# Performance work log

Hardware: AMD Instinct MI355X
Metric: run time of the kernel (lower is better)

The kernel has to match this reference:

```python
import jax, jax.numpy as jnp
import numpy as np

LAMBDA_WEIGHT = 1.0


def _soft_argmax(logits):
    # differentiable_argmax: sum_c softmax(logits)[c] * c along class dim
    nc = logits.shape[1]
    probs = jax.nn.softmax(logits, axis=1)
    idx = jnp.arange(nc, dtype=logits.dtype)[None, :, None, None]
    return jnp.sum(probs * idx, axis=1)  # [B, H, W]


def _pair_loss(mask, d):
    # mask: [L] bool over row-major flattened HxW; d: [L] float (col - row).
    # torch.where returns row-major order, coord[:,1]-coord[:,0] == d at masked
    # pixels; second diff is |d_i - d_prev| over consecutive masked pixels.
    L = mask.shape[0]
    pos = jnp.where(mask, jnp.arange(L), -1)
    last = jax.lax.cummax(pos, axis=0)                 # last masked index <= i
    prev = jnp.concatenate([jnp.full((1,), -1), last[:-1]])  # strictly before i
    valid = mask & (prev >= 0)
    dprev = d[jnp.clip(prev, 0, L - 1)]
    s = jnp.sum(jnp.where(valid, jnp.abs(d - dprev), 0.0))
    npairs = jnp.sum(valid)
    npts = jnp.sum(mask)
    mean = s / jnp.maximum(npairs, 1).astype(d.dtype)
    # N==0 contributes 0 (the `continue`); N==1 gives an empty-mean (NaN) in
    # torch -- guarded to 0 here (such degenerate classes are skipped).
    return jnp.where(npts >= 2, mean / (npts + 1).astype(d.dtype), 0.0)


def reference(logits, labels):
    bs, nc, h, w = logits.shape
    seg = jnp.floor(jax.lax.stop_gradient(_soft_argmax(logits))).astype(jnp.int32)
    seg = seg.reshape(bs, h * w)                       # [B, L] row-major
    # d[i] = col - row for flattened index i
    i = jnp.arange(h * w)
    d = ((i % w) - (i // w)).astype(jnp.float32)       # [L]
    classes = jnp.arange(1, nc, dtype=jnp.int32)       # skip background c=0
    masks = seg[:, None, :] == classes[None, :, None]  # [B, nc-1, L]
    per = jax.vmap(jax.vmap(_pair_loss, in_axes=(0, None)), in_axes=(0, None))(masks, d)
    return jnp.sum(per) * LAMBDA_WEIGHT


def setup_inputs() -> dict:
    key = jax.random.key(0)
    k1, k2 = jax.random.split(key)
    logits = jax.random.normal(k1, (16, 7, 368, 640), dtype=jnp.float32)
    labels = jax.random.randint(k2, (16, 368, 640), 0, 7, dtype=jnp.int64)
    return {"logits": logits, "labels": labels}
```

## Files before the change

kernel.cpp:

```cpp
#include <hip/hip_runtime.h>
#include <cstdint>
#include <cstddef>

#define BB 16
#define CC 7
#define HH 368
#define WW 640
#define LL (HH * WW)
#define NCLS 6
#define NCOMBO (BB * NCLS)
#define PXB 1024
#define BPB (LL / PXB)
#define NBLK (BB * BPB)

struct St { int S, cnt, first, last; };

__device__ inline St comb(const St& a, const St& b) {
    if (a.cnt == 0) return b;
    if (b.cnt == 0) return a;
    St r;
    r.S     = a.S + b.S + abs(b.first - a.last);
    r.cnt   = a.cnt + b.cnt;
    r.first = a.first;
    r.last  = b.last;
    return r;
}

__global__ __launch_bounds__(256) void fused_kernel(const float* __restrict__ logits,
                                                    int4* __restrict__ blkStates) {
    int blk = blockIdx.x;
    int b  = blk / BPB;
    int bb = blk - b * BPB;
    int t  = threadIdx.x;
    int i  = bb * PXB + t * 4;
    const float* base = logits + (size_t)b * CC * LL + i;

    float x[CC][4];
#pragma unroll
    for (int c = 0; c < CC; ++c) {
        float4 v = *reinterpret_cast<const float4*>(base + (size_t)c * LL);
        x[c][0] = v.x; x[c][1] = v.y; x[c][2] = v.z; x[c][3] = v.w;
    }

    int row = i / WW;
    int col = i - row * WW;
    int d0  = col - row;

    St st[NCLS];
#pragma unroll
    for (int c = 0; c < NCLS; ++c) { st[c].S = 0; st[c].cnt = 0; st[c].first = 0; st[c].last = 0; }

#pragma unroll
    for (int k = 0; k < 4; ++k) {
        float m = x[0][k];
#pragma unroll
        for (int c = 1; c < CC; ++c) m = fmaxf(m, x[c][k]);
        float s = 0.0f, w = 0.0f;
#pragma unroll
        for (int c = 0; c < CC; ++c) {
            float e = __expf(x[c][k] - m);
            s += e;
            w += e * (float)c;
        }
        int sv = (int)floorf(__fdividef(w, s));
        int d  = d0 + k;
#pragma unroll
        for (int c = 0; c < NCLS; ++c) {
            if (sv == c + 1) {
                if (st[c].cnt == 0) st[c].first = d;
                else                st[c].S += abs(d - st[c].last);
                st[c].last = d;
                st[c].cnt++;
            }
        }
    }

    __shared__ int4 red[NCLS][256];
#pragma unroll
    for (int c = 0; c < NCLS; ++c)
        red[c][t] = make_int4(st[c].S, st[c].cnt, st[c].first, st[c].last);
    __syncthreads();

    for (int step = 1; step < 256; step <<= 1) {
        if ((t & (2 * step - 1)) == 0) {
#pragma unroll
            for (int c = 0; c < NCLS; ++c) {
                int4 A = red[c][t], B = red[c][t + step];
                St a{A.x, A.y, A.z, A.w}, bs{B.x, B.y, B.z, B.w};
                St r = comb(a, bs);
                red[c][t] = make_int4(r.S, r.cnt, r.first, r.last);
            }
        }
        __syncthreads();
    }

    if (t < NCLS) blkStates[(size_t)blk * NCLS + t] = red[t][0];
}

__global__ __launch_bounds__(256) void combine_kernel(const int4* __restrict__ blkStates,
                                                      float* __restrict__ out) {
    int combo = blockIdx.x;
    int b = combo / NCLS;
    int c = combo - b * NCLS;
    int t = threadIdx.x;

    St st{0, 0, 0, 0};
    if (t < BPB) {
        int4 v = blkStates[(size_t)(b * BPB + t) * NCLS + c];
        st = St{v.x, v.y, v.z, v.w};
    }

    __shared__ int4 red[256];
    red[t] = make_int4(st.S, st.cnt, st.first, st.last);
    __syncthreads();

    for (int step = 1; step < 256; step <<= 1) {
        if ((t & (2 * step - 1)) == 0) {
            int4 A = red[t], B = red[t + step];
            St a{A.x, A.y, A.z, A.w}, bs{B.x, B.y, B.z, B.w};
            St r = comb(a, bs);
            red[t] = make_int4(r.S, r.cnt, r.first, r.last);
        }
        __syncthreads();
    }

    if (t == 0) {
        int n = red[0].y;
        if (n >= 2) {
            double res = ((double)red[0].x / (double)(n - 1)) / (double)(n + 1);
            atomicAdd(out, (float)res);
        }
    }
}

extern "C" void kernel_launch(void* const* d_in, const int* in_sizes, int n_in,
                              void* d_out, int out_size, void* d_ws, size_t ws_size,
                              hipStream_t stream) {
    const float* logits = (const float*)d_in[0];
    float* out = (float*)d_out;

    int4* blkStates = (int4*)d_ws;

    hipMemsetAsync(out, 0, sizeof(float) * out_size, stream);
    fused_kernel<<<NBLK, 256, 0, stream>>>(logits, blkStates);
    combine_kernel<<<NCOMBO, 256, 0, stream>>>(blkStates, out);
}
```

Baseline: 171.5 us.

## Replace shared-memory tree reductions with wavefront shuffle reductions and 16 px/thread

Each thread now processes 16 pixels with 64-thread blocks (one wavefront), and the per-class segment states are reduced with __shfl_down instead of a shared-memory tree with repeated __syncthreads. The block-state layout becomes class-major, and combine_kernel also uses shuffle reduction plus a small cross-wave step. This removes the LDS traffic and barrier overhead that dominated a memory-light kernel. The trade-off is strided per-thread loads, which may reduce coalescing.

Measured after the change: 201.5 us. +17.5%, slower.

```diff
diff --git a/kernel.cpp b/kernel.cpp
--- a/kernel.cpp
+++ b/kernel.cpp
@@ -9,38 +9,41 @@
 #define LL (HH * WW)
 #define NCLS 6
 #define NCOMBO (BB * NCLS)
-#define PXB 1024
+#define PXT 16
+#define TPB 64
+#define PXB (PXT * TPB)
 #define BPB (LL / PXB)
 #define NBLK (BB * BPB)
 
 struct St { int S, cnt, first, last; };
 
 __device__ inline St comb(const St& a, const St& b) {
-    if (a.cnt == 0) return b;
-    if (b.cnt == 0) return a;
     St r;
-    r.S     = a.S + b.S + abs(b.first - a.last);
+    int both = (a.cnt > 0) & (b.cnt > 0);
+    r.S     = a.S + b.S + (both ? abs(b.first - a.last) : 0);
     r.cnt   = a.cnt + b.cnt;
-    r.first = a.first;
-    r.last  = b.last;
+    r.first = (a.cnt > 0) ? a.first : b.first;
+    r.last  = (b.cnt > 0) ? b.last : a.last;
     return r;
 }
 
-__global__ __launch_bounds__(256) void fused_kernel(const float* __restrict__ logits,
-                                                    int4* __restrict__ blkStates) {
+__device__ inline St shfl_down_st(const St& s, int off) {
+    St r;
+    r.S     = __shfl_down(s.S, off, 64);
+    r.cnt   = __shfl_down(s.cnt, off, 64);
+    r.first = __shfl_down(s.first, off, 64);
+    r.last  = __shfl_down(s.last, off, 64);
+    return r;
+}
+
+__global__ __launch_bounds__(64) void fused_kernel(const float* __restrict__ logits,
+                                                   int4* __restrict__ blkStates) {
     int blk = blockIdx.x;
     int b  = blk / BPB;
     int bb = blk - b * BPB;
     int t  = threadIdx.x;
-    int i  = bb * PXB + t * 4;
+    int i  = bb * PXB + t * PXT;
     const float* base = logits + (size_t)b * CC * LL + i;
-
-    float x[CC][4];
-#pragma unroll
-    for (int c = 0; c < CC; ++c) {
-        float4 v = *reinterpret_cast<const float4*>(base + (size_t)c * LL);
-        x[c][0] = v.x; x[c][1] = v.y; x[c][2] = v.z; x[c][3] = v.w;
-    }
 
     int row = i / WW;
     int col = i - row * WW;
@@ -51,50 +54,55 @@
     for (int c = 0; c < NCLS; ++c) { st[c].S = 0; st[c].cnt = 0; st[c].first = 0; st[c].last = 0; }
 
 #pragma unroll
-    for (int k = 0; k < 4; ++k) {
-        float m = x[0][k];
-#pragma unroll
-        for (int c = 1; c < CC; ++c) m = fmaxf(m, x[c][k]);
-        float s = 0.0f, w = 0.0f;
+    for (int j = 0; j < PXT / 4; ++j) {
+        float x[CC][4];
 #pragma unroll
         for (int c = 0; c < CC; ++c) {
-            float e = __expf(x[c][k] - m);
-            s += e;
-            w += e * (float)c;
+            float4 v = *reinterpret_cast<const float4*>(base + (size_t)c * LL + j * 4);
+            x[c][0] = v.x; x[c][1] = v.y; x[c][2] = v.z; x[c][3] = v.w;
         }
-        int sv = (int)floorf(__fdividef(w, s));
-        int d  = d0 + k;
 #pragma unroll
-        for (int c = 0; c < NCLS; ++c) {
-            if (sv == c + 1) {
-                if (st[c].cnt == 0) st[c].first = d;
-                else                st[c].S += abs(d - st[c].last);
-                st[c].last = d;
-                st[c].cnt++;
+        for (int k = 0; k < 4; ++k) {
+            float m = x[0][k];
+#pragma unroll
+            for (int c = 1; c < CC; ++c) m = fmaxf(m, x[c][k]);
+            float s = 0.0f, w = 0.0f;
+#pragma unroll
+            for (int c = 0; c < CC; ++c) {
+                float e = __expf(x[c][k] - m);
+                s += e;
+                w += e * (float)c;
+            }
+            int sv = (int)floorf(__fdividef(w, s));
+            int d  = d0 + j * 4 + k;
+#pragma unroll
+            for (int c = 0; c < NCLS; ++c) {
+                if (sv == c + 1) {
+                    if (st[c].cnt == 0) st[c].first = d;
+                    else                st[c].S += abs(d - st[c].last);
+                    st[c].last = d;
+                    st[c].cnt++;
+                }
             }
         }
     }
 
-    __shared__ int4 red[NCLS][256];
 #pragma unroll
-    for (int c = 0; c < NCLS; ++c)
-        red[c][t] = make_int4(st[c].S, st[c].cnt, st[c].first, st[c].last);
-    __syncthreads();
-
-    for (int step = 1; step < 256; step <<= 1) {
-        if ((t & (2 * step - 1)) == 0) {
+    for (int c = 0; c < NCLS; ++c) {
+        St s = st[c];
 #pragma unroll
-            for (int c = 0; c < NCLS; ++c) {
-                int4 A = red[c][t], B = red[c][t + step];
-                St a{A.x, A.y, A.z, A.w}, bs{B.x, B.y, B.z, B.w};
-                St r = comb(a, bs);
-                red[c][t] = make_int4(r.S, r.cnt, r.first, r.last);
-            }
+        for (int off = 1; off < 64; off <<= 1) {
+            St o = shfl_down_st(s, off);
+            s = comb(s, o);
         }
-        __syncthreads();
+        st[c] = s;
     }
 
-    if (t < NCLS) blkStates[(size_t)blk * NCLS + t] = red[t][0];
+    if (t == 0) {
+#pragma unroll
+        for (int c = 0; c < NCLS; ++c)
+            blkStates[(size_t)c * NBLK + blk] = make_int4(st[c].S, st[c].cnt, st[c].first, st[c].last);
+    }
 }
 
 __global__ __launch_bounds__(256) void combine_kernel(const int4* __restrict__ blkStates,
@@ -106,28 +114,31 @@
 
     St st{0, 0, 0, 0};
     if (t < BPB) {
-        int4 v = blkStates[(size_t)(b * BPB + t) * NCLS + c];
+        int4 v = blkStates[(size_t)c * NBLK + b * BPB + t];
         st = St{v.x, v.y, v.z, v.w};
     }
 
-    __shared__ int4 red[256];
-    red[t] = make_int4(st.S, st.cnt, st.first, st.last);
+#pragma unroll
+    for (int off = 1; off < 64; off <<= 1) {
+        St o = shfl_down_st(st, off);
+        st = comb(st, o);
+    }
+
+    __shared__ int4 ws[4];
+    int wave = t >> 6;
+    if ((t & 63) == 0) ws[wave] = make_int4(st.S, st.cnt, st.first, st.last);
     __syncthreads();
 
-    for (int step = 1; step < 256; step <<= 1) {
-        if ((t & (2 * step - 1)) == 0) {
-            int4 A = red[t], B = red[t + step];
-            St a{A.x, A.y, A.z, A.w}, bs{B.x, B.y, B.z, B.w};
-            St r = comb(a, bs);
-            red[t] = make_int4(r.S, r.cnt, r.first, r.last);
+    if (t == 0) {
+        St acc{ws[0].x, ws[0].y, ws[0].z, ws[0].w};
+#pragma unroll
+        for (int w = 1; w < 4; ++w) {
+            St o{ws[w].x, ws[w].y, ws[w].z, ws[w].w};
+            acc = comb(acc, o);
         }
-        __syncthreads();
-    }
-
-    if (t == 0) {
-        int n = red[0].y;
+        int n = acc.cnt;
         if (n >= 2) {
-            double res = ((double)red[0].x / (double)(n - 1)) / (double)(n + 1);
+            double res = ((double)acc.S / (double)(n - 1)) / (double)(n + 1);
             atomicAdd(out, (float)res);
         }
     }
@@ -142,6 +153,6 @@
     int4* blkStates = (int4*)d_ws;
 
     hipMemsetAsync(out, 0, sizeof(float) * out_size, stream);
-    fused_kernel<<<NBLK, 256, 0, stream>>>(logits, blkStates);
+    fused_kernel<<<NBLK, TPB, 0, stream>>>(logits, blkStates);
     combine_kernel<<<NCOMBO, 256, 0, stream>>>(blkStates, out);
 }
```
